# Performance work log

Hardware: AMD Instinct MI355X
Metric: run time of the kernel (lower is better)

## Reference

```python
import jax, jax.numpy as jnp
import numpy as np

B, CAR_NUM, E, H, L, T, O = 4096, 32, 512, 512, 2, 60, 2


def setup_inputs():
    ks = jax.random.split(jax.random.key(0), 17)
    s = 0.02
    f = lambda k, shp: jax.random.normal(k, shp, jnp.float32) * s
    return {
        'x': jax.random.normal(ks[0], (B, 6 + CAR_NUM * 6), jnp.float32),
        'emb_main_W': f(ks[1], (E, 6)),
        'emb_main_b': f(ks[2], (E,)),
        'emb_veh_W': f(ks[3], (E, 6)),
        'emb_veh_b': f(ks[4], (E,)),
        'enc_Wih': f(ks[5], (L, H, E)),
        'enc_Whh': f(ks[6], (L, H, H)),
        'enc_bih': f(ks[7], (L, H)),
        'enc_bhh': f(ks[8], (L, H)),
        'dec_Wih': f(ks[9], (L, H, H)),
        'dec_Whh': f(ks[10], (L, H, H)),
        'dec_bih': f(ks[11], (L, H)),
        'dec_bhh': f(ks[12], (L, H)),
        'head_W1': f(ks[13], (H, H)),
        'head_b1': f(ks[14], (H,)),
        'head_W2': f(ks[15], (O, H)),
        'head_b2': f(ks[16], (O,)),
        'seq_length': T,
    }


def _cell(h_prev, inp, Wih, Whh, bih, bhh):
    # multi-layer vanilla RNN cell: h_l = tanh(W_ih x + b_ih + W_hh h + b_hh)
    hs = []
    for l in range(Wih.shape[0]):
        hl = jnp.tanh(inp @ Wih[l].T + bih[l] + h_prev[l] @ Whh[l].T + bhh[l])
        hs.append(hl)
        inp = hl
    return jnp.stack(hs), inp


def _forward(x, emb_main_W, emb_main_b, emb_veh_W, emb_veh_b,
             enc_Wih, enc_Whh, enc_bih, enc_bhh,
             dec_Wih, dec_Whh, dec_bih, dec_bhh,
             head_W1, head_b1, head_W2, head_b2, seq_length):
    Bx = x.shape[0]
    car_num = (x.shape[1] - 6) // 6
    main = x[:, :6]
    veh = x[:, 6:6 + car_num * 6].reshape(Bx, car_num, 6)
    main_emb = main @ emb_main_W.T + emb_main_b            # [B, E]
    veh_emb = veh @ emb_veh_W.T + emb_veh_b                # [B, car_num, E]
    seq = jnp.tanh(jnp.concatenate([veh_emb, main_emb[:, None, :]], axis=1))  # [B, car_num+1, E]

    h0 = jnp.zeros((enc_Wih.shape[0], Bx, enc_Whh.shape[-1]), x.dtype)

    def enc_step(h, x_t):
        h, top = _cell(h, x_t, enc_Wih, enc_Whh, enc_bih, enc_bhh)
        return h, top

    h, enc_tops = jax.lax.scan(enc_step, h0, jnp.swapaxes(seq, 0, 1))

    def head(z):
        return jnp.tanh(jax.nn.relu(z @ head_W1.T + head_b1) @ head_W2.T + head_b2)

    def dec_step(carry, _):
        h, inp = carry
        h, top = _cell(h, inp, dec_Wih, dec_Whh, dec_bih, dec_bhh)
        return (h, top), head(top)

    _, preds = jax.lax.scan(dec_step, (h, enc_tops[-1]), None, length=seq_length)
    return jnp.swapaxes(preds, 0, 1)                       # [B, seq_length, O]


def reference(x, emb_main_W, emb_main_b, emb_veh_W, emb_veh_b,
              enc_Wih, enc_Whh, enc_bih, enc_bhh,
              dec_Wih, dec_Whh, dec_bih, dec_bhh,
              head_W1, head_b1, head_W2, head_b2, seq_length):
    return _forward(x, emb_main_W, emb_main_b, emb_veh_W, emb_veh_b,
                    enc_Wih, enc_Whh, enc_bih, enc_bhh,
                    dec_Wih, dec_Whh, dec_bih, dec_bhh,
                    head_W1, head_b1, head_W2, head_b2, seq_length)
```

## Files before the change

### kernel.cpp

```cpp
#include <hip/hip_runtime.h>
#include <cstdint>
#include <cstddef>


typedef __bf16 bf16x8 __attribute__((ext_vector_type(8)));
typedef float  f32x4  __attribute__((ext_vector_type(4)));

#define SZ    262144
#define XDIM  198
#define NF    2
#define MB    32
#define NBLK  128
#define SLICE 16384

#define MFMA16(a, b, c) __builtin_amdgcn_mfma_f32_16x16x32_bf16((a), (b), (c), 0, 0, 0)
#define AS1 __attribute__((address_space(1)))
#define AS3 __attribute__((address_space(3)))

__device__ __host__ __forceinline__ unsigned short f2bf(float x) {
  uint32_t u = __builtin_bit_cast(uint32_t, x);
  u = (u + 0x7FFFu + ((u >> 16) & 1u)) >> 16;
  return (unsigned short)u;
}

__global__ void pack_w(const float* __restrict__ src, unsigned short* __restrict__ dst,
                       int N, int Ksrc, int Kpad) {
  int idx  = blockIdx.x * 256 + threadIdx.x;
  int Npad = (N + 15) & ~15;
  int total = Npad * Kpad;
  if (idx >= total) return;
  int n = idx / Kpad, k = idx - n * Kpad;
  float v = (n < N && k < Ksrc) ? src[n * Ksrc + k] : 0.f;
  int ntile = n >> 4, kstep = k >> 5, i = k & 7;
  int lane  = (((k >> 3) & 3) << 4) | (n & 15);
  int NT    = Npad >> 4;
  dst[((((kstep * NT) + ntile) * 64 + lane) << 3) + i] = f2bf(v);
}

__device__ __forceinline__ bf16x8 lds_frag(const unsigned short* buf, int m, int k) {
  int idx = m * 512 + (k ^ ((m & 7) << 3));
  return *reinterpret_cast<const bf16x8*>(buf + idx);
}

__device__ __forceinline__ void bar_sync_lds() {
  asm volatile("s_waitcnt lgkmcnt(0)" ::: "memory");
  __builtin_amdgcn_s_barrier();
  __builtin_amdgcn_sched_barrier(0);
}
__device__ __forceinline__ void bar_throttle() {
  __builtin_amdgcn_s_barrier();
  __builtin_amdgcn_sched_barrier(0);
}

__device__ __forceinline__ void stage_own(const unsigned short* __restrict__ gslice,
                                          unsigned short* lslice, int wv, int lane) {
  const unsigned short* g0 = gslice + wv * 1024 + lane * 8;
  unsigned short* l0 = lslice + wv * 1024;
  __builtin_amdgcn_global_load_lds((const AS1 void*)g0, (AS3 void*)l0, 16, 0, 0);
  __builtin_amdgcn_global_load_lds((const AS1 void*)(g0 + 512), (AS3 void*)(l0 + 512), 16, 0, 0);
}

__device__ __forceinline__ void gemm16(f32x4 acc[2][NF], const unsigned short* Abuf,
    const unsigned short* __restrict__ Wg, const unsigned short* __restrict__ Wnextg,
    unsigned short* wb0, unsigned short* wb1, int& sp, int lane, int wv) {
  const int m    = lane & 15;
  const int ksub = (lane >> 4) << 3;
  const int wreg = wv * 1024;
  bf16x8 a0 = lds_frag(Abuf, m, ksub);
  bf16x8 a1 = lds_frag(Abuf + 16 * 512, m, ksub);
  for (int ks = 0; ks < 16; ++ks) {
    bar_throttle();
    stage_own((ks < 15 ? (Wg + (ks + 1) * SLICE) : Wnextg),
              (sp ? wb0 : wb1), wv, lane);
    asm volatile("s_waitcnt vmcnt(2)" ::: "memory");
    __builtin_amdgcn_sched_barrier(0);
    const unsigned short* cur = (sp ? wb1 : wb0) + wreg;
    bf16x8 w0 = *reinterpret_cast<const bf16x8*>(cur + lane * 8);
    bf16x8 w1 = *reinterpret_cast<const bf16x8*>(cur + 512 + lane * 8);
    bf16x8 a0n = a0, a1n = a1;
    if (ks < 15) {
      a0n = lds_frag(Abuf, m, (ks + 1) * 32 + ksub);
      a1n = lds_frag(Abuf + 16 * 512, m, (ks + 1) * 32 + ksub);
    }
    acc[0][0] = MFMA16(a0, w0, acc[0][0]);
    acc[1][0] = MFMA16(a1, w0, acc[1][0]);
    acc[0][1] = MFMA16(a0, w1, acc[0][1]);
    acc[1][1] = MFMA16(a1, w1, acc[1][1]);
    a0 = a0n; a1 = a1n;
    sp ^= 1;
  }
}

__device__ __forceinline__ void init_acc2(f32x4 acc[2][NF], float b0, float b1) {
  acc[0][0] = (f32x4){b0, b0, b0, b0};
  acc[1][0] = (f32x4){b0, b0, b0, b0};
  acc[0][1] = (f32x4){b1, b1, b1, b1};
  acc[1][1] = (f32x4){b1, b1, b1, b1};
}

template <int ACT>
__device__ __forceinline__ void writeback(unsigned short* dst, const f32x4 acc[2][NF],
                                          int lane, int wv) {
#pragma unroll
  for (int mt = 0; mt < 2; ++mt) {
#pragma unroll
    for (int nf = 0; nf < NF; ++nf) {
#pragma unroll
      for (int j = 0; j < 4; ++j) {
        float v = acc[mt][nf][j];
        v = (ACT == 0) ? tanhf(v) : fmaxf(v, 0.f);
        int row = mt * 16 + ((lane >> 4) << 2) + j;
        int col = (wv * NF + nf) * 16 + (lane & 15);
        dst[row * 512 + (col ^ ((row & 7) << 3))] = f2bf(v);
      }
    }
  }
}

__global__ __launch_bounds__(1024, 4) void rnn_main(
    const float* __restrict__ x,
    const unsigned short* __restrict__ wp,
    const float* __restrict__ enc_bih, const float* __restrict__ enc_bhh,
    const float* __restrict__ dec_bih, const float* __restrict__ dec_bhh,
    const float* __restrict__ head_b1, const float* __restrict__ head_b2,
    const float* __restrict__ emb_main_b, const float* __restrict__ emb_veh_b,
    float* __restrict__ out) {
  __shared__ alignas(16) unsigned short H0[MB * 512];
  __shared__ alignas(16) unsigned short H1[MB * 512];
  __shared__ alignas(16) unsigned short INP[MB * 512];
  __shared__ alignas(16) unsigned short WBUF[2][SLICE];

  unsigned short* XA = INP;

  const int tid  = threadIdx.x;
  const int lane = tid & 63;
  const int wv   = tid >> 6;
  const int row0 = blockIdx.x * MB;
  const int wreg = wv * 1024;

  const unsigned short* encWih0 = wp + 0 * SZ;
  const unsigned short* encWih1 = wp + 1 * SZ;
  const unsigned short* encWhh0 = wp + 2 * SZ;
  const unsigned short* encWhh1 = wp + 3 * SZ;
  const unsigned short* decWih0 = wp + 4 * SZ;
  const unsigned short* decWih1 = wp + 5 * SZ;
  const unsigned short* decWhh0 = wp + 6 * SZ;
  const unsigned short* decWhh1 = wp + 7 * SZ;
  const unsigned short* headW1p = wp + 8 * SZ;
  const unsigned short* headW2p = wp + 9 * SZ;
  const unsigned short* vehp    = wp + 9 * SZ + 8192;
  const unsigned short* mainp   = wp + 9 * SZ + 8192 + 16384;

  const int c0 = (wv * NF + 0) * 16 + (lane & 15);
  const int c1 = c0 + 16;
  const float bEv0 = emb_veh_b[c0],  bEv1 = emb_veh_b[c1];
  const float bEm0 = emb_main_b[c0], bEm1 = emb_main_b[c1];
  const float bE00 = enc_bih[c0] + enc_bhh[c0];
  const float bE01 = enc_bih[c1] + enc_bhh[c1];
  const float bE10 = enc_bih[512 + c0] + enc_bhh[512 + c0];
  const float bE11 = enc_bih[512 + c1] + enc_bhh[512 + c1];
  const float bD00 = dec_bih[c0] + dec_bhh[c0];
  const float bD01 = dec_bih[c1] + dec_bhh[c1];
  const float bD10 = dec_bih[512 + c0] + dec_bhh[512 + c0];
  const float bD11 = dec_bih[512 + c1] + dec_bhh[512 + c1];
  const float bH0 = head_b1[c0], bH1 = head_b1[c1];
  const float b2v = head_b2[lane & 1];

  for (int i = tid; i < MB * 512; i += 1024) { H0[i] = 0; H1[i] = 0; }
  bar_sync_lds();

  f32x4 acc[2][NF];
  int sp = 0;
  stage_own(vehp, WBUF[0], wv, lane);

  for (int t = 0; t < 33; ++t) {
    for (int i = tid; i < MB * 48; i += 1024) XA[i] = 0;
    bar_sync_lds();
    if (tid < MB * 6) {
      int m = tid / 6, kk = tid - m * 6;
      int cx = (t < 32) ? (6 + t * 6 + kk) : kk;
      XA[m * 48 + kk] = f2bf(x[(size_t)(row0 + m) * XDIM + cx]);
    }
    bar_sync_lds();
    {
      init_acc2(acc, (t < 32) ? bEv0 : bEm0, (t < 32) ? bEv1 : bEm1);
      int m = lane & 15, ksub = (lane >> 4) << 3;
      bf16x8 a0 = *reinterpret_cast<const bf16x8*>(XA + m * 48 + ksub);
      bf16x8 a1 = *reinterpret_cast<const bf16x8*>(XA + (16 + m) * 48 + ksub);
      bar_throttle();
      stage_own(encWih0, WBUF[sp ^ 1], wv, lane);
      asm volatile("s_waitcnt vmcnt(2)" ::: "memory");
      __builtin_amdgcn_sched_barrier(0);
      const unsigned short* cur = WBUF[sp] + wreg;
      bf16x8 w0 = *reinterpret_cast<const bf16x8*>(cur + lane * 8);
      bf16x8 w1 = *reinterpret_cast<const bf16x8*>(cur + 512 + lane * 8);
      acc[0][0] = MFMA16(a0, w0, acc[0][0]);
      acc[1][0] = MFMA16(a1, w0, acc[1][0]);
      acc[0][1] = MFMA16(a0, w1, acc[0][1]);
      acc[1][1] = MFMA16(a1, w1, acc[1][1]);
      sp ^= 1;
      bar_sync_lds();
      writeback<0>(INP, acc, lane, wv);
      bar_sync_lds();
    }
    init_acc2(acc, bE00, bE01);
    gemm16(acc, INP, encWih0, encWhh0, WBUF[0], WBUF[1], sp, lane, wv);
    gemm16(acc, H0,  encWhh0, encWih1, WBUF[0], WBUF[1], sp, lane, wv);
    bar_sync_lds();
    writeback<0>(H0, acc, lane, wv);
    bar_sync_lds();
    const unsigned short* after =
        (t < 31) ? vehp : (t == 31 ? mainp : decWih0);
    init_acc2(acc, bE10, bE11);
    gemm16(acc, H0, encWih1, encWhh1, WBUF[0], WBUF[1], sp, lane, wv);
    gemm16(acc, H1, encWhh1, after,   WBUF[0], WBUF[1], sp, lane, wv);
    bar_sync_lds();
    writeback<0>(H1, acc, lane, wv);
    bar_sync_lds();
  }

  for (int t = 0; t < 60; ++t) {
    init_acc2(acc, bD00, bD01);
    gemm16(acc, H1, decWih0, decWhh0, WBUF[0], WBUF[1], sp, lane, wv);
    gemm16(acc, H0, decWhh0, decWih1, WBUF[0], WBUF[1], sp, lane, wv);
    bar_sync_lds();
    writeback<0>(H0, acc, lane, wv);
    bar_sync_lds();
    init_acc2(acc, bD10, bD11);
    gemm16(acc, H0, decWih1, decWhh1, WBUF[0], WBUF[1], sp, lane, wv);
    gemm16(acc, H1, decWhh1, headW1p, WBUF[0], WBUF[1], sp, lane, wv);
    bar_sync_lds();
    writeback<0>(H1, acc, lane, wv);
    bar_sync_lds();
    init_acc2(acc, bH0, bH1);
    gemm16(acc, H1, headW1p, decWih0, WBUF[0], WBUF[1], sp, lane, wv);
    bar_sync_lds();
    writeback<1>(INP, acc, lane, wv);
    bar_sync_lds();

    if (wv < 2) {
      const unsigned short* A2 = INP + wv * 16 * 512;
      int m = lane & 15, ksub = (lane >> 4) << 3;
      f32x4 a2[4];
#pragma unroll
      for (int c = 0; c < 4; ++c) a2[c] = (f32x4){0.f, 0.f, 0.f, 0.f};
#pragma unroll
      for (int ks = 0; ks < 16; ++ks) {
        bf16x8 a = lds_frag(A2, m, ks * 32 + ksub);
        const bf16x8* bp =
            reinterpret_cast<const bf16x8*>(headW2p + (ks * 64 + lane) * 8);
        a2[ks & 3] = MFMA16(a, *bp, a2[ks & 3]);
      }
      f32x4 s = a2[0] + a2[1] + a2[2] + a2[3];
      if (m < 2) {
#pragma unroll
        for (int j = 0; j < 4; ++j) {
          int r = row0 + wv * 16 + ((lane >> 4) << 2) + j;
          out[(size_t)r * 120 + t * 2 + m] = tanhf(s[j] + b2v);
        }
      }
    }
  }
  asm volatile("s_waitcnt vmcnt(0)" ::: "memory");
}

extern "C" void kernel_launch(void* const* d_in, const int* in_sizes, int n_in,
                              void* d_out, int out_size, void* d_ws, size_t ws_size,
                              hipStream_t stream) {
  const float* x          = (const float*)d_in[0];
  const float* emb_main_W = (const float*)d_in[1];
  const float* emb_main_b = (const float*)d_in[2];
  const float* emb_veh_W  = (const float*)d_in[3];
  const float* emb_veh_b  = (const float*)d_in[4];
  const float* enc_Wih    = (const float*)d_in[5];
  const float* enc_Whh    = (const float*)d_in[6];
  const float* enc_bih    = (const float*)d_in[7];
  const float* enc_bhh    = (const float*)d_in[8];
  const float* dec_Wih    = (const float*)d_in[9];
  const float* dec_Whh    = (const float*)d_in[10];
  const float* dec_bih    = (const float*)d_in[11];
  const float* dec_bhh    = (const float*)d_in[12];
  const float* head_W1    = (const float*)d_in[13];
  const float* head_b1    = (const float*)d_in[14];
  const float* head_W2    = (const float*)d_in[15];
  const float* head_b2    = (const float*)d_in[16];

  unsigned short* wp = (unsigned short*)d_ws;

  dim3 blk(256);
  auto P = [&](const float* src, unsigned short* dst) {
    hipLaunchKernelGGL(pack_w, dim3(1024), blk, 0, stream, src, dst, 512, 512, 512);
  };
  P(enc_Wih + 0 * SZ, wp + 0 * SZ);
  P(enc_Wih + 1 * SZ, wp + 1 * SZ);
  P(enc_Whh + 0 * SZ, wp + 2 * SZ);
  P(enc_Whh + 1 * SZ, wp + 3 * SZ);
  P(dec_Wih + 0 * SZ, wp + 4 * SZ);
  P(dec_Wih + 1 * SZ, wp + 5 * SZ);
  P(dec_Whh + 0 * SZ, wp + 6 * SZ);
  P(dec_Whh + 1 * SZ, wp + 7 * SZ);
  P(head_W1, wp + 8 * SZ);
  hipLaunchKernelGGL(pack_w, dim3(32), blk, 0, stream, head_W2, wp + 9 * SZ, 2, 512, 512);
  hipLaunchKernelGGL(pack_w, dim3(64), blk, 0, stream, emb_veh_W, wp + 9 * SZ + 8192, 512, 6, 32);
  hipLaunchKernelGGL(pack_w, dim3(64), blk, 0, stream, emb_main_W, wp + 9 * SZ + 8192 + 16384, 512, 6, 32);

  hipLaunchKernelGGL(rnn_main, dim3(NBLK), dim3(1024), 0, stream,
                     x, (const unsigned short*)wp, enc_bih, enc_bhh, dec_bih, dec_bhh,
                     head_b1, head_b2, emb_main_b, emb_veh_b, (float*)d_out);
}
```

Measured before the change: 2.534 ms.

## Load weight fragments directly into registers instead of staging through LDS

Weight fragments are no longer staged into a double-buffered LDS slice with global_load_lds. Each wave now loads its own bf16x8 fragments straight into registers, using a 4-deep ring prefetched two k-steps ahead with explicit vmcnt waits. This frees 64KB of LDS and drops the LDS write and read round trip for weights. In exchange, the cross-GEMM prefetch of the next matrix is lost, so each GEMM start now exposes load latency. Register pressure also rises.

```diff
diff --git a/kernel.cpp b/kernel.cpp
--- a/kernel.cpp
+++ b/kernel.cpp
@@ -14,8 +14,6 @@
 #define SLICE 16384
 
 #define MFMA16(a, b, c) __builtin_amdgcn_mfma_f32_16x16x32_bf16((a), (b), (c), 0, 0, 0)
-#define AS1 __attribute__((address_space(1)))
-#define AS3 __attribute__((address_space(3)))
 
 __device__ __host__ __forceinline__ unsigned short f2bf(float x) {
   uint32_t u = __builtin_bit_cast(uint32_t, x);
@@ -52,31 +50,39 @@
   __builtin_amdgcn_sched_barrier(0);
 }
 
-__device__ __forceinline__ void stage_own(const unsigned short* __restrict__ gslice,
-                                          unsigned short* lslice, int wv, int lane) {
-  const unsigned short* g0 = gslice + wv * 1024 + lane * 8;
-  unsigned short* l0 = lslice + wv * 1024;
-  __builtin_amdgcn_global_load_lds((const AS1 void*)g0, (AS3 void*)l0, 16, 0, 0);
-  __builtin_amdgcn_global_load_lds((const AS1 void*)(g0 + 512), (AS3 void*)(l0 + 512), 16, 0, 0);
+__device__ __forceinline__ bf16x8 ld_w0(const unsigned short* p) {
+  bf16x8 w;
+  asm volatile("global_load_dwordx4 %0, %1, off" : "=v"(w) : "v"(p) : "memory");
+  return w;
+}
+__device__ __forceinline__ bf16x8 ld_w1(const unsigned short* p) {
+  bf16x8 w;
+  asm volatile("global_load_dwordx4 %0, %1, off offset:1024" : "=v"(w) : "v"(p) : "memory");
+  return w;
 }
 
 __device__ __forceinline__ void gemm16(f32x4 acc[2][NF], const unsigned short* Abuf,
-    const unsigned short* __restrict__ Wg, const unsigned short* __restrict__ Wnextg,
-    unsigned short* wb0, unsigned short* wb1, int& sp, int lane, int wv) {
+    const unsigned short* __restrict__ Wg, int lane, int wv) {
   const int m    = lane & 15;
   const int ksub = (lane >> 4) << 3;
-  const int wreg = wv * 1024;
+  const unsigned short* base = Wg + wv * 1024 + lane * 8;
+  bf16x8 rw0[4], rw1[4];
+  rw0[0] = ld_w0(base);          rw1[0] = ld_w1(base);
+  rw0[1] = ld_w0(base + SLICE);  rw1[1] = ld_w1(base + SLICE);
   bf16x8 a0 = lds_frag(Abuf, m, ksub);
   bf16x8 a1 = lds_frag(Abuf + 16 * 512, m, ksub);
+#pragma unroll
   for (int ks = 0; ks < 16; ++ks) {
     bar_throttle();
-    stage_own((ks < 15 ? (Wg + (ks + 1) * SLICE) : Wnextg),
-              (sp ? wb0 : wb1), wv, lane);
-    asm volatile("s_waitcnt vmcnt(2)" ::: "memory");
+    if (ks < 14) {
+      rw0[(ks + 2) & 3] = ld_w0(base + (ks + 2) * SLICE);
+      rw1[(ks + 2) & 3] = ld_w1(base + (ks + 2) * SLICE);
+    }
+    if (ks < 14)       asm volatile("s_waitcnt vmcnt(4)" ::: "memory");
+    else if (ks == 14) asm volatile("s_waitcnt vmcnt(2)" ::: "memory");
+    else               asm volatile("s_waitcnt vmcnt(0)" ::: "memory");
     __builtin_amdgcn_sched_barrier(0);
-    const unsigned short* cur = (sp ? wb1 : wb0) + wreg;
-    bf16x8 w0 = *reinterpret_cast<const bf16x8*>(cur + lane * 8);
-    bf16x8 w1 = *reinterpret_cast<const bf16x8*>(cur + 512 + lane * 8);
+    bf16x8 w0 = rw0[ks & 3], w1 = rw1[ks & 3];
     bf16x8 a0n = a0, a1n = a1;
     if (ks < 15) {
       a0n = lds_frag(Abuf, m, (ks + 1) * 32 + ksub);
@@ -87,7 +93,6 @@
     acc[0][1] = MFMA16(a0, w1, acc[0][1]);
     acc[1][1] = MFMA16(a1, w1, acc[1][1]);
     a0 = a0n; a1 = a1n;
-    sp ^= 1;
   }
 }
 
@@ -128,7 +133,6 @@
   __shared__ alignas(16) unsigned short H0[MB * 512];
   __shared__ alignas(16) unsigned short H1[MB * 512];
   __shared__ alignas(16) unsigned short INP[MB * 512];
-  __shared__ alignas(16) unsigned short WBUF[2][SLICE];
 
   unsigned short* XA = INP;
 
@@ -136,7 +140,6 @@
   const int lane = tid & 63;
   const int wv   = tid >> 6;
   const int row0 = blockIdx.x * MB;
-  const int wreg = wv * 1024;
 
   const unsigned short* encWih0 = wp + 0 * SZ;
   const unsigned short* encWih1 = wp + 1 * SZ;
@@ -170,8 +173,6 @@
   bar_sync_lds();
 
   f32x4 acc[2][NF];
-  int sp = 0;
-  stage_own(vehp, WBUF[0], wv, lane);
 
   for (int t = 0; t < 33; ++t) {
     for (int i = tid; i < MB * 48; i += 1024) XA[i] = 0;
@@ -183,37 +184,32 @@
     }
     bar_sync_lds();
     {
+      const unsigned short* eb = ((t < 32) ? vehp : mainp) + wv * 1024 + lane * 8;
+      bf16x8 w0 = ld_w0(eb);
+      bf16x8 w1 = ld_w1(eb);
       init_acc2(acc, (t < 32) ? bEv0 : bEm0, (t < 32) ? bEv1 : bEm1);
       int m = lane & 15, ksub = (lane >> 4) << 3;
       bf16x8 a0 = *reinterpret_cast<const bf16x8*>(XA + m * 48 + ksub);
       bf16x8 a1 = *reinterpret_cast<const bf16x8*>(XA + (16 + m) * 48 + ksub);
-      bar_throttle();
-      stage_own(encWih0, WBUF[sp ^ 1], wv, lane);
-      asm volatile("s_waitcnt vmcnt(2)" ::: "memory");
+      asm volatile("s_waitcnt vmcnt(0)" ::: "memory");
       __builtin_amdgcn_sched_barrier(0);
-      const unsigned short* cur = WBUF[sp] + wreg;
-      bf16x8 w0 = *reinterpret_cast<const bf16x8*>(cur + lane * 8);
-      bf16x8 w1 = *reinterpret_cast<const bf16x8*>(cur + 512 + lane * 8);
       acc[0][0] = MFMA16(a0, w0, acc[0][0]);
       acc[1][0] = MFMA16(a1, w0, acc[1][0]);
       acc[0][1] = MFMA16(a0, w1, acc[0][1]);
       acc[1][1] = MFMA16(a1, w1, acc[1][1]);
-      sp ^= 1;
       bar_sync_lds();
       writeback<0>(INP, acc, lane, wv);
       bar_sync_lds();
     }
     init_acc2(acc, bE00, bE01);
-    gemm16(acc, INP, encWih0, encWhh0, WBUF[0], WBUF[1], sp, lane, wv);
-    gemm16(acc, H0,  encWhh0, encWih1, WBUF[0], WBUF[1], sp, lane, wv);
+    gemm16(acc, INP, encWih0, lane, wv);
+    gemm16(acc, H0,  encWhh0, lane, wv);
     bar_sync_lds();
     writeback<0>(H0, acc, lane, wv);
     bar_sync_lds();
-    const unsigned short* after =
-        (t < 31) ? vehp : (t == 31 ? mainp : decWih0);
     init_acc2(acc, bE10, bE11);
-    gemm16(acc, H0, encWih1, encWhh1, WBUF[0], WBUF[1], sp, lane, wv);
-    gemm16(acc, H1, encWhh1, after,   WBUF[0], WBUF[1], sp, lane, wv);
+    gemm16(acc, H0, encWih1, lane, wv);
+    gemm16(acc, H1, encWhh1, lane, wv);
     bar_sync_lds();
     writeback<0>(H1, acc, lane, wv);
     bar_sync_lds();
@@ -221,19 +217,19 @@
 
   for (int t = 0; t < 60; ++t) {
     init_acc2(acc, bD00, bD01);
-    gemm16(acc, H1, decWih0, decWhh0, WBUF[0], WBUF[1], sp, lane, wv);
-    gemm16(acc, H0, decWhh0, decWih1, WBUF[0], WBUF[1], sp, lane, wv);
+    gemm16(acc, H1, decWih0, lane, wv);
+    gemm16(acc, H0, decWhh0, lane, wv);
     bar_sync_lds();
     writeback<0>(H0, acc, lane, wv);
     bar_sync_lds();
     init_acc2(acc, bD10, bD11);
-    gemm16(acc, H0, decWih1, decWhh1, WBUF[0], WBUF[1], sp, lane, wv);
-    gemm16(acc, H1, decWhh1, headW1p, WBUF[0], WBUF[1], sp, lane, wv);
+    gemm16(acc, H0, decWih1, lane, wv);
+    gemm16(acc, H1, decWhh1, lane, wv);
     bar_sync_lds();
     writeback<0>(H1, acc, lane, wv);
     bar_sync_lds();
     init_acc2(acc, bH0, bH1);
-    gemm16(acc, H1, headW1p, decWih0, WBUF[0], WBUF[1], sp, lane, wv);
+    gemm16(acc, H1, headW1p, lane, wv);
     bar_sync_lds();
     writeback<1>(INP, acc, lane, wv);
     bar_sync_lds();
```

After: 5.586 ms. 120% more time.
